# Optimization experiments

Hardware: AMD Instinct MI355X
Metric: run time of the kernel (lower is better)

The kernel has to match this reference:

```python
import jax, jax.numpy as jnp
import numpy as np
from functools import partial

# dims
BATCH, L, H = 1, 512, 2048
NH, HD = 64, 64            # num heads, head dim
INTER = NH * HD            # 4096
G, N = 4, 64               # n_groups, ssm state size
K = 4                      # conv kernel
CONV = INTER + 2 * G * N   # 4608
PROJ = INTER + CONV + NH   # z, xBC, dt
EPS = 1e-5


def rmsnorm(x, w, eps=EPS):
    xf = x.astype(jnp.float32)
    v = jnp.mean(xf * xf, axis=-1, keepdims=True)
    return (xf * jax.lax.rsqrt(v + eps)).astype(x.dtype) * w


def setup_inputs() -> dict:
    key = jax.random.key(0)
    ks = jax.random.split(key, 12)
    rn = lambda k, s, sc=1.0: sc * jax.random.normal(k, s, dtype=jnp.float32)
    return {
        "hidden_states": rn(ks[0], (BATCH, L, H)),
        "residual": rn(ks[1], (BATCH, L, H)),
        "norm_w": 1.0 + rn(ks[2], (H,), 0.02),
        "in_proj_w": rn(ks[3], (H, PROJ), 0.02),
        "conv_w": rn(ks[4], (CONV, K), 0.2),
        "conv_b": rn(ks[5], (CONV,), 0.02),
        "A_log": jnp.log(jax.random.uniform(ks[6], (NH,), minval=1.0, maxval=16.0)),
        "dt_bias": rn(ks[7], (NH,), 0.5),
        "D": rn(ks[8], (NH,), 0.5),
        "gn_w": 1.0 + rn(ks[9], (INTER,), 0.02),
        "out_proj_w": rn(ks[10], (INTER, H), 0.02),
    }


def reference(hidden_states, residual, norm_w, in_proj_w, conv_w, conv_b,
              A_log, dt_bias, D, gn_w, out_proj_w):
    B_ = hidden_states.shape[0]
    # fused add + RMSNorm (residual is not None path)
    x = hidden_states + residual
    new_residual = x
    hs = rmsnorm(x, norm_w)

    # in_proj: [B,L,H] -> [B,L,PROJ] split into z | xBC | dt
    proj = jnp.einsum('blh,hp->blp', hs, in_proj_w)
    z = proj[..., :INTER]
    xBC = proj[..., INTER:INTER + CONV]
    dt = proj[..., INTER + CONV:]

    # causal depthwise conv of width K, then SiLU
    xp = jnp.pad(xBC, ((0, 0), (K - 1, 0), (0, 0)))
    conv = sum(xp[:, k:k + L, :] * conv_w[None, None, :, k] for k in range(K))
    xBC = jax.nn.silu(conv + conv_b)

    xh = xBC[..., :INTER].reshape(B_, L, NH, HD)
    Bm = xBC[..., INTER:INTER + G * N].reshape(B_, L, G, N)
    Cm = xBC[..., INTER + G * N:].reshape(B_, L, G, N)

    dt = jax.nn.softplus(dt + dt_bias)          # [B,L,NH]
    A = -jnp.exp(A_log)                         # [NH]
    dA = jnp.exp(dt * A)                        # [B,L,NH]

    hpg = NH // G
    Bh = jnp.repeat(Bm, hpg, axis=2)            # [B,L,NH,N]
    Ch = jnp.repeat(Cm, hpg, axis=2)

    def step(h, inp):
        dA_t, dt_t, x_t, B_t, C_t = inp
        # h: [B,NH,HD,N]
        h = h * dA_t[:, :, None, None] + (dt_t[:, :, None] * x_t)[..., None] * B_t[:, :, None, :]
        y = jnp.einsum('bhdn,bhn->bhd', h, C_t)
        return h, y

    h0 = jnp.zeros((B_, NH, HD, N), dtype=jnp.float32)
    xs = (jnp.moveaxis(dA, 1, 0), jnp.moveaxis(dt, 1, 0), jnp.moveaxis(xh, 1, 0),
          jnp.moveaxis(Bh, 1, 0), jnp.moveaxis(Ch, 1, 0))
    _, ys = jax.lax.scan(step, h0, xs)          # [L,B,NH,HD]
    y = jnp.moveaxis(ys, 0, 1) + xh * D[None, None, :, None]
    y = y.reshape(B_, L, INTER)

    # gated RMSNorm then out_proj
    y = rmsnorm(y * jax.nn.silu(z), gn_w)
    out = jnp.einsum('bli,ih->blh', y, out_proj_w)
    return out, new_residual
```

## Files before the change

kernel.cpp:

```cpp
#include <hip/hip_runtime.h>
#include <stdint.h>

#define LSEQ 512
#define HDIM 2048
#define NH 64
#define HD 64
#define INTER 4096
#define NG 4
#define NSTATE 64
#define CONVC 4608
#define PROJC 8768
#define EPS 1e-5f
#define CL 64
#define NC 8
#define NHDN (NH * HD * NSTATE)

typedef __attribute__((ext_vector_type(8))) short bf16x8;
typedef __attribute__((ext_vector_type(4))) short short4v;
typedef __attribute__((ext_vector_type(4))) float f32x4;

__device__ __forceinline__ short f2bf(float f) {
  union { float f; uint32_t u; } v; v.f = f;
  uint32_t r = v.u + 0x7FFFu + ((v.u >> 16) & 1u);
  return (short)(r >> 16);
}

__device__ __forceinline__ uint32_t cvt_pk_bf16(float lo, float hi) {
  uint32_t r;
  asm("v_cvt_pk_bf16_f32 %0, %1, %2" : "=v"(r) : "v"(lo), "v"(hi));
  return r;
}

__device__ __forceinline__ float bf2f(short s) {
  union { uint32_t u; float f; } v; v.u = ((uint32_t)(uint16_t)s) << 16;
  return v.f;
}

__device__ __forceinline__ float siluf(float v) {
  return v / (1.f + expf(-v));
}

__device__ __forceinline__ int xcd_swizzle(int orig, int nwg) {
  int q = nwg >> 3, r = nwg & 7;
  int xcd = orig & 7, idx = orig >> 3;
  return (xcd < r ? xcd * (q + 1) : r * (q + 1) + (xcd - r) * q) + idx;
}

__global__ __launch_bounds__(256) void k_add_rmsnorm(
    const float* __restrict__ hid, const float* __restrict__ res,
    const float* __restrict__ w, float* __restrict__ resid_out,
    short* __restrict__ hsb) {
  __shared__ float sred[4];
  const int row = blockIdx.x, tid = threadIdx.x;
  const float4* h4 = (const float4*)(hid + (size_t)row * HDIM);
  const float4* r4 = (const float4*)(res + (size_t)row * HDIM);
  float4* ro4 = (float4*)(resid_out + (size_t)row * HDIM);
  float4 a0 = h4[tid], b0 = r4[tid];
  float4 a1 = h4[tid + 256], b1 = r4[tid + 256];
  float4 xa, xb;
  xa.x = a0.x + b0.x; xa.y = a0.y + b0.y; xa.z = a0.z + b0.z; xa.w = a0.w + b0.w;
  xb.x = a1.x + b1.x; xb.y = a1.y + b1.y; xb.z = a1.z + b1.z; xb.w = a1.w + b1.w;
  ro4[tid] = xa; ro4[tid + 256] = xb;
  float ss = xa.x*xa.x + xa.y*xa.y + xa.z*xa.z + xa.w*xa.w
           + xb.x*xb.x + xb.y*xb.y + xb.z*xb.z + xb.w*xb.w;
  #pragma unroll
  for (int off = 32; off >= 1; off >>= 1) ss += __shfl_down(ss, off);
  if ((tid & 63) == 0) sred[tid >> 6] = ss;
  __syncthreads();
  float tot = sred[0] + sred[1] + sred[2] + sred[3];
  float rs = rsqrtf(tot / (float)HDIM + EPS);
  int e0 = tid * 4, e1 = (tid + 256) * 4;
  short4v s0, s1;
  s0.x = f2bf(xa.x * rs * w[e0+0]); s0.y = f2bf(xa.y * rs * w[e0+1]);
  s0.z = f2bf(xa.z * rs * w[e0+2]); s0.w = f2bf(xa.w * rs * w[e0+3]);
  s1.x = f2bf(xb.x * rs * w[e1+0]); s1.y = f2bf(xb.y * rs * w[e1+1]);
  s1.z = f2bf(xb.z * rs * w[e1+2]); s1.w = f2bf(xb.w * rs * w[e1+3]);
  *(short4v*)(hsb + (size_t)row * HDIM + e0) = s0;
  *(short4v*)(hsb + (size_t)row * HDIM + e1) = s1;
}

__global__ __launch_bounds__(256) void k_transpose_cvt(
    const float* __restrict__ src, short* __restrict__ dst, int R, int C) {
  __shared__ float tile[32][33];
  const int tx = threadIdx.x & 31, ty = threadIdx.x >> 5;
  const int c0 = blockIdx.x * 32, r0 = blockIdx.y * 32;
  #pragma unroll
  for (int i = 0; i < 4; ++i)
    tile[ty + i*8][tx] = src[(size_t)(r0 + ty + i*8) * C + c0 + tx];
  __syncthreads();
  #pragma unroll
  for (int i = 0; i < 4; ++i)
    dst[(size_t)(c0 + ty + i*8) * R + r0 + tx] = f2bf(tile[tx][ty + i*8]);
}

__global__ __launch_bounds__(256) void k_gemm1(
    const short* __restrict__ A, const float* __restrict__ Bw,
    short* __restrict__ zbf, short* __restrict__ xbc,
    float* __restrict__ dtf) {
  constexpr int BM = 128, MR = 4, WROWS = 64;
  const int M = LSEQ, N = PROJC, K = HDIM;
  __shared__ short lA[2][BM * 64];
  __shared__ short lB[64 * 64];
  const int tid = threadIdx.x, lane = tid & 63, wid = tid >> 6;

  const int NMB = M / BM, NNB = N / 64;
  const int nwg = NMB * NNB;
  int wg = xcd_swizzle(blockIdx.x, nwg);
  const int mi = wg % NMB;
  const int ni = wg / NMB;
  const int m0 = mi * BM, n0 = ni * 64;
  const int wm = wid >> 1, wn = wid & 1;

  const int lrow8 = lane >> 3;
  const int cswz = ((lane & 7) ^ lrow8) * 8;

  auto stageA = [&](int buf, int kt) {
    #pragma unroll
    for (int r2 = 0; r2 < MR; ++r2) {
      int idx = r2 * 4 + wid;
      __builtin_amdgcn_global_load_lds(
          (const __attribute__((address_space(1))) int*)(A + (size_t)(m0 + idx * 8 + lrow8) * K + kt + cswz),
          (__attribute__((address_space(3))) int*)(&lA[buf][idx * 512]),
          16, 0, 0);
    }
  };

  float breg[16];
  auto loadB = [&](int kt) {
    #pragma unroll
    for (int r = 0; r < 2; ++r)
      #pragma unroll
      for (int j = 0; j < 8; ++j)
        breg[r * 8 + j] = Bw[(size_t)(kt + wid * 16 + r * 8 + j) * N + n0 + lane];
  };
  auto writeB = [&]() {
    #pragma unroll
    for (int r = 0; r < 2; ++r) {
      uint4 v;
      v.x = cvt_pk_bf16(breg[r*8+0], breg[r*8+1]);
      v.y = cvt_pk_bf16(breg[r*8+2], breg[r*8+3]);
      v.z = cvt_pk_bf16(breg[r*8+4], breg[r*8+5]);
      v.w = cvt_pk_bf16(breg[r*8+6], breg[r*8+7]);
      int ko = wid * 2 + r;
      *(uint4*)&lB[lane * 64 + ((ko ^ (lane & 7)) << 3)] = v;
    }
  };

  f32x4 acc[MR][2] = {};
  const int lrow = lane & 15, lkb = (lane >> 4) * 8;
  const int NT = K >> 6;
  loadB(0);
  stageA(0, 0);
  writeB();
  asm volatile("s_waitcnt vmcnt(0)" ::: "memory");
  asm volatile("s_waitcnt lgkmcnt(0)" ::: "memory");
  __builtin_amdgcn_s_barrier();
  for (int t = 0; t < NT; ++t) {
    int cur = t & 1;
    if (t + 1 < NT) {
      loadB((t + 1) * 64);
      stageA(cur ^ 1, (t + 1) * 64);
    }
    #pragma unroll
    for (int kk = 0; kk < 2; ++kk) {
      bf16x8 a[MR], b[2];
      #pragma unroll
      for (int m = 0; m < MR; ++m) {
        int row = wm * WROWS + m * 16 + lrow;
        int colel = (kk * 32 + lkb) ^ ((row & 7) << 3);
        a[m] = *(const bf16x8*)&lA[cur][row * 64 + colel];
      }
      #pragma unroll
      for (int n = 0; n < 2; ++n) {
        int row = wn * 32 + n * 16 + lrow;
        int colel = (kk * 32 + lkb) ^ ((row & 7) << 3);
        b[n] = *(const bf16x8*)&lB[row * 64 + colel];
      }
      #pragma unroll
      for (int m = 0; m < MR; ++m)
        #pragma unroll
        for (int n = 0; n < 2; ++n)
          acc[m][n] = __builtin_amdgcn_mfma_f32_16x16x32_bf16(a[m], b[n], acc[m][n], 0, 0, 0);
    }
    __builtin_amdgcn_s_barrier();
    if (t + 1 < NT) writeB();
    asm volatile("s_waitcnt vmcnt(0)" ::: "memory");
    asm volatile("s_waitcnt lgkmcnt(0)" ::: "memory");
    __builtin_amdgcn_s_barrier();
  }
  #pragma unroll
  for (int m = 0; m < MR; ++m) {
    int row = m0 + wm * WROWS + m * 16 + (lane >> 4) * 4;
    #pragma unroll
    for (int n = 0; n < 2; ++n) {
      int coll = wn * 32 + n * 16 + (lane & 15);
      #pragma unroll
      for (int r = 0; r < 4; ++r) {
        float v = acc[m][n][r];
        if (ni < 64)
          zbf[(size_t)(row + r) * INTER + n0 + coll] = f2bf(v);
        else if (ni < 136)
          xbc[(size_t)(row + r) * CONVC + (n0 - INTER) + coll] = f2bf(v);
        else
          dtf[(row + r) * 64 + coll] = v;
      }
    }
  }
}

template <int BM, int KS>
__global__ __launch_bounds__(256) void k_gemm_bf16(
    const short* __restrict__ A, const short* __restrict__ B,
    float* __restrict__ C, int M, int N, int K) {
  __shared__ short lA[2][BM * 64];
  __shared__ short lB[2][64 * 64];
  const int tid = threadIdx.x;
  const int lane = tid & 63, wid = tid >> 6;
  constexpr int MR = BM / 32;
  constexpr int WROWS = BM / 2;

  const int NMB = M / BM, NNB = N / 64;
  const int nwg = NMB * NNB * KS;
  int wg = xcd_swizzle(blockIdx.x, nwg);
  const int mi = wg % NMB;
  int rest = wg / NMB;
  const int zi = (KS > 1) ? (rest % KS) : 0;
  const int ni = (KS > 1) ? (rest / KS) : rest;
  const int m0 = mi * BM, n0 = ni * 64;
  const int wm = wid >> 1, wn = wid & 1;

  const int lrow8 = lane >> 3;
  const int cswz = ((lane & 7) ^ lrow8) * 8;

  const int Kc = K / KS;
  const int kbase = zi * Kc;
  float* Cp = C + (size_t)zi * M * N;

  auto stage = [&](int buf, int kt) {
    #pragma unroll
    for (int r2 = 0; r2 < MR; ++r2) {
      int idx = r2 * 4 + wid;
      __builtin_amdgcn_global_load_lds(
          (const __attribute__((address_space(1))) int*)(A + (size_t)(m0 + idx * 8 + lrow8) * K + kt + cswz),
          (__attribute__((address_space(3))) int*)(&lA[buf][idx * 512]),
          16, 0, 0);
    }
    #pragma unroll
    for (int r2 = 0; r2 < 2; ++r2) {
      int idx = r2 * 4 + wid;
      __builtin_amdgcn_global_load_lds(
          (const __attribute__((address_space(1))) int*)(B + (size_t)(n0 + idx * 8 + lrow8) * K + kt + cswz),
          (__attribute__((address_space(3))) int*)(&lB[buf][idx * 512]),
          16, 0, 0);
    }
  };

  f32x4 acc[MR][2] = {};
  const int lrow = lane & 15, lkb = (lane >> 4) * 8;
  const int NT = Kc >> 6;
  stage(0, kbase);
  for (int t = 0; t < NT; ++t) {
    int cur = t & 1;
    if (t + 1 < NT) {
      stage(cur ^ 1, kbase + (t + 1) * 64);
      if constexpr (MR == 2) asm volatile("s_waitcnt vmcnt(4)" ::: "memory");
      else                   asm volatile("s_waitcnt vmcnt(6)" ::: "memory");
    } else {
      asm volatile("s_waitcnt vmcnt(0)" ::: "memory");
    }
    __builtin_amdgcn_s_barrier();
    #pragma unroll
    for (int kk = 0; kk < 2; ++kk) {
      bf16x8 a[MR], b[2];
      #pragma unroll
      for (int m = 0; m < MR; ++m) {
        int row = wm * WROWS + m * 16 + lrow;
        int colel = (kk * 32 + lkb) ^ ((row & 7) << 3);
        a[m] = *(const bf16x8*)&lA[cur][row * 64 + colel];
      }
      #pragma unroll
      for (int n = 0; n < 2; ++n) {
        int row = wn * 32 + n * 16 + lrow;
        int colel = (kk * 32 + lkb) ^ ((row & 7) << 3);
        b[n] = *(const bf16x8*)&lB[cur][row * 64 + colel];
      }
      #pragma unroll
      for (int m = 0; m < MR; ++m)
        #pragma unroll
        for (int n = 0; n < 2; ++n)
          acc[m][n] = __builtin_amdgcn_mfma_f32_16x16x32_bf16(a[m], b[n], acc[m][n], 0, 0, 0);
    }
    __builtin_amdgcn_s_barrier();
  }
  #pragma unroll
  for (int m = 0; m < MR; ++m) {
    int row = m0 + wm * WROWS + m * 16 + (lane >> 4) * 4;
    int col = n0 + wn * 32 + (lane & 15);
    #pragma unroll
    for (int n = 0; n < 2; ++n)
      #pragma unroll
      for (int r = 0; r < 4; ++r)
        Cp[(size_t)(row + r) * N + col + n * 16] = acc[m][n][r];
  }
}

__global__ __launch_bounds__(256) void k_reduce4(
    const float* __restrict__ p, float* __restrict__ out, int n) {
  int i = (blockIdx.x * 256 + threadIdx.x) * 4;
  float4 a = *(const float4*)(p + i);
  float4 b = *(const float4*)(p + n + i);
  float4 c = *(const float4*)(p + 2 * (size_t)n + i);
  float4 d = *(const float4*)(p + 3 * (size_t)n + i);
  float4 o;
  o.x = (a.x + b.x) + (c.x + d.x);
  o.y = (a.y + b.y) + (c.y + d.y);
  o.z = (a.z + b.z) + (c.z + d.z);
  o.w = (a.w + b.w) + (c.w + d.w);
  *(float4*)(out + i) = o;
}

__global__ __launch_bounds__(256) void k_conv(
    const short* __restrict__ xbc, const float* __restrict__ dtf,
    const float* __restrict__ cw, const float* __restrict__ cb,
    const float* __restrict__ A_log, const float* __restrict__ dt_bias,
    short* __restrict__ convo, float* __restrict__ dtb,
    float* __restrict__ ldab) {
  const int l0 = blockIdx.y * 64;
  if (blockIdx.x == CONVC / 256) {
    #pragma unroll
    for (int i = 0; i < 16; ++i) {
      int idx = threadIdx.x + i * 256;
      int l = l0 + (idx >> 6), h = idx & 63;
      float v = dtf[l * 64 + h] + dt_bias[h];
      float dt = v > 20.f ? v : log1pf(expf(v));
      float lda = dt * (-expf(A_log[h]));
      dtb[h * LSEQ + l] = dt;
      ldab[h * LSEQ + l] = lda;
    }
    return;
  }
  const int c = blockIdx.x * 256 + threadIdx.x;
  const float w0 = cw[c*4+0], w1 = cw[c*4+1], w2 = cw[c*4+2], w3 = cw[c*4+3];
  const float bias = cb[c];
  float x0 = 0.f, x1 = 0.f, x2 = 0.f;
  if (l0 > 0) {
    x0 = bf2f(xbc[(size_t)(l0-3) * CONVC + c]);
    x1 = bf2f(xbc[(size_t)(l0-2) * CONVC + c]);
    x2 = bf2f(xbc[(size_t)(l0-1) * CONVC + c]);
  }
  for (int l = l0; l < l0 + 64; ++l) {
    float x3 = bf2f(xbc[(size_t)l * CONVC + c]);
    float accv = bias + x0*w0 + x1*w1 + x2*w2 + x3*w3;
    convo[(size_t)l * CONVC + c] = f2bf(siluf(accv));
    x0 = x1; x1 = x2; x2 = x3;
  }
}

__global__ __launch_bounds__(256) void k_ssd(
    const short* __restrict__ convo, const float* __restrict__ dtb,
    const float* __restrict__ ldab, const float* __restrict__ Dp,
    short* __restrict__ ybuf, float* __restrict__ hend,
    float* __restrict__ Pbuf, float* __restrict__ cdbuf) {
  __shared__ __align__(16) short Xt[64 * 72];
  __shared__ __align__(16) short Bs[64 * 72];
  __shared__ __align__(16) short Cs[64 * 72];
  __shared__ __align__(16) short Btw[64 * 72];
  __shared__ __align__(16) short Ms[64 * 72];
  __shared__ float s_s[64], s_dt[64], s_w[64];
  const int c = blockIdx.x, head = blockIdx.y;
  const int g = head >> 4;
  const int tid = threadIdx.x, lane = tid & 63, wid = tid >> 6;
  const int l0 = c * CL;
  const short* xbase = convo + (size_t)l0 * CONVC + head * HD;
  const short* Bbase = convo + (size_t)l0 * CONVC + INTER + g * NSTATE;
  const short* Cbase = convo + (size_t)l0 * CONVC + INTER + NG * NSTATE + g * NSTATE;

  if (tid < 64) {
    float ps = ldab[head * LSEQ + l0 + tid];
    #pragma unroll
    for (int o = 1; o < 64; o <<= 1) {
      float u = __shfl_up(ps, o);
      if (tid >= o) ps += u;
    }
    float dtv = dtb[head * LSEQ + l0 + tid];
    s_s[tid] = ps;
    s_dt[tid] = dtv;
    float s63 = __shfl(ps, 63);
    s_w[tid] = __expf(s63 - ps) * dtv;
    cdbuf[head * LSEQ + l0 + tid] = __expf(ps);
    if (tid == 63) Pbuf[c * NH + head] = __expf(ps);
  }
  #pragma unroll
  for (int rep = 0; rep < 4; ++rep) {
    int l = (tid >> 4) + rep * 16;
    int d = (tid & 15) * 4;
    size_t roff = (size_t)l * CONVC;
    short4v xv = *(const short4v*)(xbase + roff + d);
    Xt[(d + 0) * 72 + l] = xv.x;
    Xt[(d + 1) * 72 + l] = xv.y;
    Xt[(d + 2) * 72 + l] = xv.z;
    Xt[(d + 3) * 72 + l] = xv.w;
    *(short4v*)&Bs[l * 72 + d] = *(const short4v*)(Bbase + roff + d);
    *(short4v*)&Cs[l * 72 + d] = *(const short4v*)(Cbase + roff + d);
  }
  __syncthreads();
  #pragma unroll
  for (int rep = 0; rep < 16; ++rep) {
    int idx = rep * 256 + tid;
    int l = idx >> 6, n = idx & 63;
    Btw[n * 72 + l] = f2bf(bf2f(Bs[l * 72 + n]) * s_w[l]);
  }
  __syncthreads();
  const int lrow = lane & 15, lkb = (lane >> 4) * 8;
  f32x4 sacc[4] = {};
  f32x4 hacc[4] = {};
  #pragma unroll
  for (int kk = 0; kk < 2; ++kk) {
    bf16x8 ac = *(const bf16x8*)&Cs[(wid * 16 + lrow) * 72 + kk * 32 + lkb];
    bf16x8 ax = *(const bf16x8*)&Xt[(wid * 16 + lrow) * 72 + kk * 32 + lkb];
    #pragma unroll
    for (int t4 = 0; t4 < 4; ++t4) {
      bf16x8 bb = *(const bf16x8*)&Bs[(t4 * 16 + lrow) * 72 + kk * 32 + lkb];
      bf16x8 bw = *(const bf16x8*)&Btw[(t4 * 16 + lrow) * 72 + kk * 32 + lkb];
      sacc[t4] = __builtin_amdgcn_mfma_f32_16x16x32_bf16(ac, bb, sacc[t4], 0, 0, 0);
      hacc[t4] = __builtin_amdgcn_mfma_f32_16x16x32_bf16(ax, bw, hacc[t4], 0, 0, 0);
    }
  }
  float* hb = hend + ((size_t)c * NH + head) * (HD * NSTATE);
  #pragma unroll
  for (int t4 = 0; t4 < 4; ++t4) {
    int j = t4 * 16 + lrow;
    float sj = s_s[j], dtj = s_dt[j];
    #pragma unroll
    for (int r = 0; r < 4; ++r) {
      int i = wid * 16 + (lane >> 4) * 4 + r;
      float m = (j <= i) ? __expf(s_s[i] - sj) * dtj * sacc[t4][r] : 0.f;
      Ms[i * 72 + j] = f2bf(m);
      hb[i * NSTATE + j] = hacc[t4][r];
    }
  }
  __syncthreads();
  f32x4 yacc[4] = {};
  #pragma unroll
  for (int kk = 0; kk < 2; ++kk) {
    bf16x8 am = *(const bf16x8*)&Ms[(wid * 16 + lrow) * 72 + kk * 32 + lkb];
    #pragma unroll
    for (int t4 = 0; t4 < 4; ++t4) {
      bf16x8 bx = *(const bf16x8*)&Xt[(t4 * 16 + lrow) * 72 + kk * 32 + lkb];
      yacc[t4] = __builtin_amdgcn_mfma_f32_16x16x32_bf16(am, bx, yacc[t4], 0, 0, 0);
    }
  }
  const float Dv = Dp[head];
  #pragma unroll
  for (int t4 = 0; t4 < 4; ++t4) {
    int d = t4 * 16 + lrow;
    #pragma unroll
    for (int r = 0; r < 4; ++r) {
      int i = wid * 16 + (lane >> 4) * 4 + r;
      float xv = bf2f(Xt[d * 72 + i]);
      ybuf[(size_t)(l0 + i) * INTER + head * HD + d] = f2bf(yacc[t4][r] + xv * Dv);
    }
  }
}

__global__ __launch_bounds__(256) void k_scan_combine(
    const float* __restrict__ hend, const float* __restrict__ Pbuf,
    float* __restrict__ hinbuf) {
  const int e = blockIdx.x * 256 + threadIdx.x;
  const int head = e >> 12;
  float h = 0.f;
  #pragma unroll
  for (int c = 1; c < NC; ++c) {
    h = Pbuf[(c - 1) * NH + head] * h + hend[(size_t)(c - 1) * NHDN + e];
    hinbuf[(size_t)c * NHDN + e] = h;
  }
}

__global__ __launch_bounds__(256) void k_scan_fixup(
    const short* __restrict__ convo, const float* __restrict__ hinbuf,
    const float* __restrict__ cdbuf, short* __restrict__ ybuf) {
  __shared__ float sh[NSTATE][HD + 1];
  __shared__ float sc[CL][NSTATE];
  __shared__ float scd[CL];
  const int bid = blockIdx.x;
  const int c = (bid >> 6) + 1, head = bid & 63, g = head >> 4;
  const int t = threadIdx.x;
  #pragma unroll
  for (int i = 0; i < 16; ++i) {
    int idx = t + i * 256;
    int d = idx >> 6, n = idx & 63;
    sh[n][d] = hinbuf[(size_t)c * NHDN + head * (HD * NSTATE) + idx];
  }
  #pragma unroll
  for (int i = 0; i < 16; ++i) {
    int idx = t + i * 256;
    int ll = idx >> 6, n = idx & 63;
    sc[ll][n] = bf2f(convo[(size_t)(c * CL + ll) * CONVC + INTER + NG * NSTATE + g * NSTATE + n]);
  }
  if (t < CL) scd[t] = cdbuf[head * LSEQ + c * CL + t];
  __syncthreads();
  const int d = t & 63, w = t >> 6;
  #pragma unroll
  for (int i = 0; i < 4; ++i) {
    int l0 = i * 16 + w * 4;
    float a0 = 0.f, a1 = 0.f, a2 = 0.f, a3 = 0.f;
    for (int n = 0; n < NSTATE; ++n) {
      float hv = sh[n][d];
      a0 += hv * sc[l0 + 0][n];
      a1 += hv * sc[l0 + 1][n];
      a2 += hv * sc[l0 + 2][n];
      a3 += hv * sc[l0 + 3][n];
    }
    size_t base = (size_t)(c * CL + l0) * INTER + head * HD + d;
    ybuf[base + 0 * INTER] = f2bf(bf2f(ybuf[base + 0 * INTER]) + scd[l0 + 0] * a0);
    ybuf[base + 1 * INTER] = f2bf(bf2f(ybuf[base + 1 * INTER]) + scd[l0 + 1] * a1);
    ybuf[base + 2 * INTER] = f2bf(bf2f(ybuf[base + 2 * INTER]) + scd[l0 + 2] * a2);
    ybuf[base + 3 * INTER] = f2bf(bf2f(ybuf[base + 3 * INTER]) + scd[l0 + 3] * a3);
  }
}

__global__ __launch_bounds__(256) void k_gated_norm(
    const short* __restrict__ ybuf, const short* __restrict__ zbf,
    const float* __restrict__ gw, short* __restrict__ y2b) {
  __shared__ float sred[4];
  const int row = blockIdx.x, tid = threadIdx.x;
  const short4v* y4 = (const short4v*)(ybuf + (size_t)row * INTER);
  const short4v* z4 = (const short4v*)(zbf + (size_t)row * INTER);
  float g[16];
  float ss = 0.f;
  #pragma unroll
  for (int i = 0; i < 4; ++i) {
    short4v y = y4[tid + i * 256];
    short4v z = z4[tid + i * 256];
    float g0 = bf2f(y.x) * siluf(bf2f(z.x)), g1 = bf2f(y.y) * siluf(bf2f(z.y));
    float g2 = bf2f(y.z) * siluf(bf2f(z.z)), g3 = bf2f(y.w) * siluf(bf2f(z.w));
    g[i*4+0] = g0; g[i*4+1] = g1; g[i*4+2] = g2; g[i*4+3] = g3;
    ss += g0*g0 + g1*g1 + g2*g2 + g3*g3;
  }
  #pragma unroll
  for (int off = 32; off >= 1; off >>= 1) ss += __shfl_down(ss, off);
  if ((tid & 63) == 0) sred[tid >> 6] = ss;
  __syncthreads();
  float tot = sred[0] + sred[1] + sred[2] + sred[3];
  float rs = rsqrtf(tot / (float)INTER + EPS);
  #pragma unroll
  for (int i = 0; i < 4; ++i) {
    int e = (tid + i * 256) * 4;
    short4v s;
    s.x = f2bf(g[i*4+0] * rs * gw[e+0]);
    s.y = f2bf(g[i*4+1] * rs * gw[e+1]);
    s.z = f2bf(g[i*4+2] * rs * gw[e+2]);
    s.w = f2bf(g[i*4+3] * rs * gw[e+3]);
    *(short4v*)(y2b + (size_t)row * INTER + e) = s;
  }
}

extern "C" void kernel_launch(void* const* d_in, const int* in_sizes, int n_in,
                              void* d_out, int out_size, void* d_ws, size_t ws_size,
                              hipStream_t stream) {
  const float* hid     = (const float*)d_in[0];
  const float* res     = (const float*)d_in[1];
  const float* norm_w  = (const float*)d_in[2];
  const float* w1      = (const float*)d_in[3];
  const float* cw      = (const float*)d_in[4];
  const float* cb      = (const float*)d_in[5];
  const float* A_log   = (const float*)d_in[6];
  const float* dt_bias = (const float*)d_in[7];
  const float* Dp      = (const float*)d_in[8];
  const float* gw      = (const float*)d_in[9];
  const float* w2      = (const float*)d_in[10];

  float* out = (float*)d_out;
  float* resid_out = out + (size_t)LSEQ * HDIM;

  char* ws = (char*)d_ws;
  short* hsb  = (short*)(ws);
  float* hend   = (float*)(ws + 2097152);
  float* p2     = (float*)(ws + 2097152);
  float* hinbuf = (float*)(ws + 10485760);
  float* Pbuf   = (float*)(ws + 18874368);
  float* cdbuf  = (float*)(ws + 18876416);
  short* zbf  = (short*)(ws + 38010880);
  short* xbc  = (short*)(ws + 42205184);
  float* dtf  = (float*)(ws + 46923776);
  short* convo= (short*)(ws + 55967744);
  float* dtb  = (float*)(ws + 65404928);
  float* ldab = (float*)(ws + 65536000);
  short* ybuf = (short*)(ws + 65667072);
  short* y2b  = (short*)(ws + 74055680);
  short* w2t  = (short*)(ws + 78249984);

  k_add_rmsnorm<<<LSEQ, 256, 0, stream>>>(hid, res, norm_w, resid_out, hsb);
  k_gemm1<<<(LSEQ/128)*(PROJC/64), 256, 0, stream>>>(hsb, w1, zbf, xbc, dtf);
  k_conv<<<dim3(CONVC/256 + 1, NC), 256, 0, stream>>>(xbc, dtf, cw, cb, A_log, dt_bias, convo, dtb, ldab);
  k_ssd<<<dim3(NC, NH), 256, 0, stream>>>(convo, dtb, ldab, Dp, ybuf, hend, Pbuf, cdbuf);
  k_scan_combine<<<NHDN/256, 256, 0, stream>>>(hend, Pbuf, hinbuf);
  k_scan_fixup<<<(NC-1)*NH, 256, 0, stream>>>(convo, hinbuf, cdbuf, ybuf);
  k_gated_norm<<<LSEQ, 256, 0, stream>>>(ybuf, zbf, gw, y2b);
  k_transpose_cvt<<<dim3(HDIM/32, INTER/32), 256, 0, stream>>>(w2, w2t, INTER, HDIM);
  k_gemm_bf16<64, 4><<<(LSEQ/64)*(HDIM/64)*4, 256, 0, stream>>>(y2b, w2t, p2, LSEQ, HDIM, INTER);
  k_reduce4<<<LSEQ*HDIM/1024, 256, 0, stream>>>(p2, out, LSEQ*HDIM);
}
```

Before: 130.1 us.

## Pre-transpose in_proj weight to bf16 and stage both GEMM operands via direct LDS loads

```diff
diff --git a/kernel.cpp b/kernel.cpp
--- a/kernel.cpp
+++ b/kernel.cpp
@@ -23,12 +23,6 @@
   union { float f; uint32_t u; } v; v.f = f;
   uint32_t r = v.u + 0x7FFFu + ((v.u >> 16) & 1u);
   return (short)(r >> 16);
-}
-
-__device__ __forceinline__ uint32_t cvt_pk_bf16(float lo, float hi) {
-  uint32_t r;
-  asm("v_cvt_pk_bf16_f32 %0, %1, %2" : "=v"(r) : "v"(lo), "v"(hi));
-  return r;
 }
 
 __device__ __forceinline__ float bf2f(short s) {
@@ -93,14 +87,14 @@
     dst[(size_t)(c0 + ty + i*8) * R + r0 + tx] = f2bf(tile[tx][ty + i*8]);
 }
 
-__global__ __launch_bounds__(256) void k_gemm1(
-    const short* __restrict__ A, const float* __restrict__ Bw,
+__global__ __launch_bounds__(256) void k_gemm1t(
+    const short* __restrict__ A, const short* __restrict__ B,
     short* __restrict__ zbf, short* __restrict__ xbc,
     float* __restrict__ dtf) {
   constexpr int BM = 128, MR = 4, WROWS = 64;
   const int M = LSEQ, N = PROJC, K = HDIM;
   __shared__ short lA[2][BM * 64];
-  __shared__ short lB[64 * 64];
+  __shared__ short lB[2][64 * 64];
   const int tid = threadIdx.x, lane = tid & 63, wid = tid >> 6;
 
   const int NMB = M / BM, NNB = N / 64;
@@ -114,7 +108,7 @@
   const int lrow8 = lane >> 3;
   const int cswz = ((lane & 7) ^ lrow8) * 8;
 
-  auto stageA = [&](int buf, int kt) {
+  auto stage = [&](int buf, int kt) {
     #pragma unroll
     for (int r2 = 0; r2 < MR; ++r2) {
       int idx = r2 * 4 + wid;
@@ -123,44 +117,29 @@
           (__attribute__((address_space(3))) int*)(&lA[buf][idx * 512]),
           16, 0, 0);
     }
-  };
-
-  float breg[16];
-  auto loadB = [&](int kt) {
-    #pragma unroll
-    for (int r = 0; r < 2; ++r)
-      #pragma unroll
-      for (int j = 0; j < 8; ++j)
-        breg[r * 8 + j] = Bw[(size_t)(kt + wid * 16 + r * 8 + j) * N + n0 + lane];
-  };
-  auto writeB = [&]() {
-    #pragma unroll
-    for (int r = 0; r < 2; ++r) {
-      uint4 v;
-      v.x = cvt_pk_bf16(breg[r*8+0], breg[r*8+1]);
-      v.y = cvt_pk_bf16(breg[r*8+2], breg[r*8+3]);
-      v.z = cvt_pk_bf16(breg[r*8+4], breg[r*8+5]);
-      v.w = cvt_pk_bf16(breg[r*8+6], breg[r*8+7]);
-      int ko = wid * 2 + r;
-      *(uint4*)&lB[lane * 64 + ((ko ^ (lane & 7)) << 3)] = v;
+    #pragma unroll
+    for (int r2 = 0; r2 < 2; ++r2) {
+      int idx = r2 * 4 + wid;
+      __builtin_amdgcn_global_load_lds(
+          (const __attribute__((address_space(1))) int*)(B + (size_t)(n0 + idx * 8 + lrow8) * K + kt + cswz),
+          (__attribute__((address_space(3))) int*)(&lB[buf][idx * 512]),
+          16, 0, 0);
     }
   };
 
   f32x4 acc[MR][2] = {};
   const int lrow = lane & 15, lkb = (lane >> 4) * 8;
   const int NT = K >> 6;
-  loadB(0);
-  stageA(0, 0);
-  writeB();
-  asm volatile("s_waitcnt vmcnt(0)" ::: "memory");
-  asm volatile("s_waitcnt lgkmcnt(0)" ::: "memory");
-  __builtin_amdgcn_s_barrier();
+  stage(0, 0);
   for (int t = 0; t < NT; ++t) {
     int cur = t & 1;
     if (t + 1 < NT) {
-      loadB((t + 1) * 64);
-      stageA(cur ^ 1, (t + 1) * 64);
-    }
+      stage(cur ^ 1, (t + 1) * 64);
+      asm volatile("s_waitcnt vmcnt(6)" ::: "memory");
+    } else {
+      asm volatile("s_waitcnt vmcnt(0)" ::: "memory");
+    }
+    __builtin_amdgcn_s_barrier();
     #pragma unroll
     for (int kk = 0; kk < 2; ++kk) {
       bf16x8 a[MR], b[2];
@@ -174,7 +153,7 @@
       for (int n = 0; n < 2; ++n) {
         int row = wn * 32 + n * 16 + lrow;
         int colel = (kk * 32 + lkb) ^ ((row & 7) << 3);
-        b[n] = *(const bf16x8*)&lB[row * 64 + colel];
+        b[n] = *(const bf16x8*)&lB[cur][row * 64 + colel];
       }
       #pragma unroll
       for (int m = 0; m < MR; ++m)
@@ -182,10 +161,6 @@
         for (int n = 0; n < 2; ++n)
           acc[m][n] = __builtin_amdgcn_mfma_f32_16x16x32_bf16(a[m], b[n], acc[m][n], 0, 0, 0);
     }
-    __builtin_amdgcn_s_barrier();
-    if (t + 1 < NT) writeB();
-    asm volatile("s_waitcnt vmcnt(0)" ::: "memory");
-    asm volatile("s_waitcnt lgkmcnt(0)" ::: "memory");
     __builtin_amdgcn_s_barrier();
   }
   #pragma unroll
@@ -575,6 +550,7 @@
 
   char* ws = (char*)d_ws;
   short* hsb  = (short*)(ws);
+  short* w1t    = (short*)(ws + 2097152);
   float* hend   = (float*)(ws + 2097152);
   float* p2     = (float*)(ws + 2097152);
   float* hinbuf = (float*)(ws + 10485760);
@@ -591,7 +567,8 @@
   short* w2t  = (short*)(ws + 78249984);
 
   k_add_rmsnorm<<<LSEQ, 256, 0, stream>>>(hid, res, norm_w, resid_out, hsb);
-  k_gemm1<<<(LSEQ/128)*(PROJC/64), 256, 0, stream>>>(hsb, w1, zbf, xbc, dtf);
+  k_transpose_cvt<<<dim3(PROJC/32, HDIM/32), 256, 0, stream>>>(w1, w1t, HDIM, PROJC);
+  k_gemm1t<<<(LSEQ/128)*(PROJC/64), 256, 0, stream>>>(hsb, w1t, zbf, xbc, dtf);
   k_conv<<<dim3(CONVC/256 + 1, NC), 256, 0, stream>>>(xbc, dtf, cw, cb, A_log, dt_bias, convo, dtb, ldab);
   k_ssd<<<dim3(NC, NH), 256, 0, stream>>>(convo, dtb, ldab, Dp, ybuf, hend, Pbuf, cdbuf);
   k_scan_combine<<<NHDN/256, 256, 0, stream>>>(hend, Pbuf, hinbuf);
```

Measured after the change: 137.6 us. 1.06x slower.

## Split in_proj GEMM along K into two partials with a reduce-and-route kernel

Applied to the files above, without the earlier changes.

```diff
diff --git a/kernel.cpp b/kernel.cpp
--- a/kernel.cpp
+++ b/kernel.cpp
@@ -95,21 +95,24 @@
 
 __global__ __launch_bounds__(256) void k_gemm1(
     const short* __restrict__ A, const float* __restrict__ Bw,
-    short* __restrict__ zbf, short* __restrict__ xbc,
-    float* __restrict__ dtf) {
-  constexpr int BM = 128, MR = 4, WROWS = 64;
+    float* __restrict__ P) {
+  constexpr int BM = 128, MR = 4, WROWS = 64, KS = 2;
   const int M = LSEQ, N = PROJC, K = HDIM;
   __shared__ short lA[2][BM * 64];
   __shared__ short lB[64 * 64];
   const int tid = threadIdx.x, lane = tid & 63, wid = tid >> 6;
 
-  const int NMB = M / BM, NNB = N / 64;
-  const int nwg = NMB * NNB;
+  const int NMB = M / BM;
+  const int nwg = NMB * (N / 64) * KS;
   int wg = xcd_swizzle(blockIdx.x, nwg);
   const int mi = wg % NMB;
-  const int ni = wg / NMB;
+  int rest = wg / NMB;
+  const int zi = rest & 1;
+  const int ni = rest >> 1;
   const int m0 = mi * BM, n0 = ni * 64;
   const int wm = wid >> 1, wn = wid & 1;
+  const int kbase = zi * (K / KS);
+  float* Pp = P + (size_t)zi * M * N;
 
   const int lrow8 = lane >> 3;
   const int cswz = ((lane & 7) ^ lrow8) * 8;
@@ -148,9 +151,9 @@
 
   f32x4 acc[MR][2] = {};
   const int lrow = lane & 15, lkb = (lane >> 4) * 8;
-  const int NT = K >> 6;
-  loadB(0);
-  stageA(0, 0);
+  const int NT = (K / KS) >> 6;
+  loadB(kbase);
+  stageA(0, kbase);
   writeB();
   asm volatile("s_waitcnt vmcnt(0)" ::: "memory");
   asm volatile("s_waitcnt lgkmcnt(0)" ::: "memory");
@@ -158,8 +161,8 @@
   for (int t = 0; t < NT; ++t) {
     int cur = t & 1;
     if (t + 1 < NT) {
-      loadB((t + 1) * 64);
-      stageA(cur ^ 1, (t + 1) * 64);
+      loadB(kbase + (t + 1) * 64);
+      stageA(cur ^ 1, kbase + (t + 1) * 64);
     }
     #pragma unroll
     for (int kk = 0; kk < 2; ++kk) {
@@ -193,18 +196,33 @@
     int row = m0 + wm * WROWS + m * 16 + (lane >> 4) * 4;
     #pragma unroll
     for (int n = 0; n < 2; ++n) {
-      int coll = wn * 32 + n * 16 + (lane & 15);
-      #pragma unroll
-      for (int r = 0; r < 4; ++r) {
-        float v = acc[m][n][r];
-        if (ni < 64)
-          zbf[(size_t)(row + r) * INTER + n0 + coll] = f2bf(v);
-        else if (ni < 136)
-          xbc[(size_t)(row + r) * CONVC + (n0 - INTER) + coll] = f2bf(v);
-        else
-          dtf[(row + r) * 64 + coll] = v;
-      }
-    }
+      int col = n0 + wn * 32 + n * 16 + (lane & 15);
+      #pragma unroll
+      for (int r = 0; r < 4; ++r)
+        Pp[(size_t)(row + r) * N + col] = acc[m][n][r];
+    }
+  }
+}
+
+__global__ __launch_bounds__(256) void k_reduce_route(
+    const float* __restrict__ p, short* __restrict__ zbf,
+    short* __restrict__ xbc, float* __restrict__ dtf) {
+  const int i = (blockIdx.x * 256 + threadIdx.x) * 4;
+  float4 a = *(const float4*)(p + i);
+  float4 b = *(const float4*)(p + (size_t)LSEQ * PROJC + i);
+  float4 o;
+  o.x = a.x + b.x; o.y = a.y + b.y; o.z = a.z + b.z; o.w = a.w + b.w;
+  const int row = i / PROJC, col = i % PROJC;
+  if (col < INTER) {
+    short4v s;
+    s.x = f2bf(o.x); s.y = f2bf(o.y); s.z = f2bf(o.z); s.w = f2bf(o.w);
+    *(short4v*)(zbf + (size_t)row * INTER + col) = s;
+  } else if (col < INTER + CONVC) {
+    short4v s;
+    s.x = f2bf(o.x); s.y = f2bf(o.y); s.z = f2bf(o.z); s.w = f2bf(o.w);
+    *(short4v*)(xbc + (size_t)row * CONVC + (col - INTER)) = s;
+  } else {
+    *(float4*)(dtf + row * 64 + (col - INTER - CONVC)) = o;
   }
 }
 
@@ -575,6 +593,7 @@
 
   char* ws = (char*)d_ws;
   short* hsb  = (short*)(ws);
+  float* p1     = (float*)(ws + 2097152);
   float* hend   = (float*)(ws + 2097152);
   float* p2     = (float*)(ws + 2097152);
   float* hinbuf = (float*)(ws + 10485760);
@@ -591,7 +610,8 @@
   short* w2t  = (short*)(ws + 78249984);
 
   k_add_rmsnorm<<<LSEQ, 256, 0, stream>>>(hid, res, norm_w, resid_out, hsb);
-  k_gemm1<<<(LSEQ/128)*(PROJC/64), 256, 0, stream>>>(hsb, w1, zbf, xbc, dtf);
+  k_gemm1<<<(LSEQ/128)*(PROJC/64)*2, 256, 0, stream>>>(hsb, w1, p1);
+  k_reduce_route<<<LSEQ*PROJC/1024, 256, 0, stream>>>(p1, zbf, xbc, dtf);
   k_conv<<<dim3(CONVC/256 + 1, NC), 256, 0, stream>>>(xbc, dtf, cw, cb, A_log, dt_bias, convo, dtb, ldab);
   k_ssd<<<dim3(NC, NH), 256, 0, stream>>>(convo, dtb, ldab, Dp, ybuf, hend, Pbuf, cdbuf);
   k_scan_combine<<<NHDN/256, 256, 0, stream>>>(hend, Pbuf, hinbuf);
```

New measurement: 136.3 us. +4.8%, slower.
